# Performance work log

Measured on AMD Instinct MI355X. Metric: run time of the kernel, lower is better.

## Reference

```python
import jax, jax.numpy as jnp
import numpy as np

N, E, F_IN, H = 10000, 20000, 128, 8
C1, C2 = 512, 256          # per-head channels: head_dim1*8, head_dim2*8
B, OUT = 64, 10            # graphs per batch, output_dim


def _lin(k, fi, fo):
    return (jax.random.normal(k, (fi, fo), jnp.float32) / np.sqrt(fi)).astype(jnp.float32)


def setup_inputs() -> dict:
    key = jax.random.key(0)
    ks = jax.random.split(key, 24)
    inp = {
        "x": jax.random.normal(ks[0], (N, F_IN), jnp.float32),
        "edge_index": jax.random.randint(ks[1], (2, E), 0, N),
        "batch": jnp.sort(jax.random.randint(ks[2], (N,), 0, B)),
        # conv1 (in=F_IN, per-head C1, H heads)
        "Wq1": _lin(ks[3], F_IN, H * C1), "bq1": 0.01 * jax.random.normal(ks[4], (H * C1,)),
        "Wk1": _lin(ks[5], F_IN, H * C1), "bk1": 0.01 * jax.random.normal(ks[6], (H * C1,)),
        "Wv1": _lin(ks[7], F_IN, H * C1), "bv1": 0.01 * jax.random.normal(ks[8], (H * C1,)),
        "Ws1": _lin(ks[9], F_IN, C1), "bs1": 0.01 * jax.random.normal(ks[10], (C1,)),
        # conv2 (in=C1, per-head C2)
        "Wq2": _lin(ks[11], C1, H * C2), "bq2": 0.01 * jax.random.normal(ks[12], (H * C2,)),
        "Wk2": _lin(ks[13], C1, H * C2), "bk2": 0.01 * jax.random.normal(ks[14], (H * C2,)),
        "Wv2": _lin(ks[15], C1, H * C2), "bv2": 0.01 * jax.random.normal(ks[16], (H * C2,)),
        "Ws2": _lin(ks[17], C1, C2), "bs2": 0.01 * jax.random.normal(ks[18], (C2,)),
        # GlobalAttention gate and final fc
        "Wg": _lin(ks[19], C2, 1), "bg": jnp.zeros((1,), jnp.float32),
        "Wf": _lin(ks[20], C2, OUT), "bf": 0.01 * jax.random.normal(ks[21], (OUT,)),
    }
    return inp


def _segment_softmax(alpha, idx, n):
    # numerically-stable softmax over variable-size segments (PyG softmax)
    amax = jax.ops.segment_max(alpha, idx, num_segments=n)
    amax = jnp.where(jnp.isfinite(amax), amax, 0.0)
    e = jnp.exp(alpha - amax[idx])
    denom = jax.ops.segment_sum(e, idx, num_segments=n)
    return e / (denom[idx] + 1e-16)


def _transformer_conv(x, edge_index, Wq, bq, Wk, bk, Wv, bv, Ws, bs, C):
    n = x.shape[0]
    src, dst = edge_index[0], edge_index[1]  # message flows src -> dst
    q = (x @ Wq + bq).reshape(n, H, C)
    k = (x @ Wk + bk).reshape(n, H, C)
    v = (x @ Wv + bv).reshape(n, H, C)
    # per-edge multi-head attention logits [E, H]
    alpha = jnp.einsum('ehc,ehc->eh', q[dst], k[src]) / np.sqrt(C).astype(np.float32)
    a = _segment_softmax(alpha, dst, n)                       # [E, H]
    out = jax.ops.segment_sum(a[:, :, None] * v[src], dst, num_segments=n)  # [N, H, C]
    out = out.mean(axis=1)                                    # concat=False -> head mean
    return out + x @ Ws + bs                                  # root/skip connection


def reference(x, edge_index, batch,
              Wq1, bq1, Wk1, bk1, Wv1, bv1, Ws1, bs1,
              Wq2, bq2, Wk2, bk2, Wv2, bv2, Ws2, bs2,
              Wg, bg, Wf, bf):
    h = jax.nn.elu(_transformer_conv(x, edge_index, Wq1, bq1, Wk1, bk1, Wv1, bv1, Ws1, bs1, C1))
    h = jax.nn.elu(_transformer_conv(h, edge_index, Wq2, bq2, Wk2, bk2, Wv2, bv2, Ws2, bs2, C2))
    # GlobalAttention pooling: gate softmax within each graph, weighted sum
    gate = _segment_softmax((h @ Wg + bg)[:, 0], batch, B)    # [N]
    g = jax.ops.segment_sum(gate[:, None] * h, batch, num_segments=B)  # [B, C2]
    return g @ Wf + bf
```

## Files before the change

### kernel.cpp

```cpp
#include <hip/hip_runtime.h>
#include <math.h>

#define NN 10000
#define NE 20000
#define FIN 128
#define NHEAD 8
#define C1 512
#define C2 256
#define NB 64
#define NOUT 10

typedef _Float16 half8v __attribute__((ext_vector_type(8)));
typedef _Float16 half4v __attribute__((ext_vector_type(4)));
typedef _Float16 half2v __attribute__((ext_vector_type(2)));
typedef float f32x4 __attribute__((ext_vector_type(4)));

template<int VEC> struct VecT;
template<> struct VecT<2> { using T = half2v; };
template<> struct VecT<4> { using T = half4v; };
template<> struct VecT<8> { using T = half8v; };

__device__ __forceinline__ unsigned enc_f(float f) {
    unsigned u = __float_as_uint(f);
    return (u & 0x80000000u) ? ~u : (u | 0x80000000u);
}
__device__ __forceinline__ float dec_f(unsigned e) {
    return (e & 0x80000000u) ? __uint_as_float(e & 0x7fffffffu) : __uint_as_float(~e);
}

__global__ void cvt_f16(const float* __restrict__ in, _Float16* __restrict__ out, int n) {
    int i = blockIdx.x * blockDim.x + threadIdx.x;
    if (i < n) out[i] = (_Float16)in[i];
}

__global__ void transpose_cvt(const float* __restrict__ W, _Float16* __restrict__ Wt,
                              int K, int N) {
    __shared__ float tile[32][33];
    int n0 = blockIdx.x * 32, k0 = blockIdx.y * 32;
    int tx = threadIdx.x, ty = threadIdx.y;
    for (int j = ty; j < 32; j += 8) tile[j][tx] = W[(size_t)(k0 + j) * N + n0 + tx];
    __syncthreads();
    for (int j = ty; j < 32; j += 8)
        Wt[(size_t)(n0 + j) * K + k0 + tx] = (_Float16)tile[tx][j];
}

__global__ void transpose_stack(const float* __restrict__ Wv, _Float16* __restrict__ Bt,
                                int Cin, int Cout) {
    __shared__ float tile[32][33];
    int h = blockIdx.z;
    int c0 = blockIdx.x * 32, k0 = blockIdx.y * 32;
    int tx = threadIdx.x, ty = threadIdx.y;
    for (int j = ty; j < 32; j += 8)
        tile[j][tx] = Wv[(size_t)(k0 + j) * (NHEAD * Cout) + (size_t)h * Cout + c0 + tx];
    __syncthreads();
    for (int j = ty; j < 32; j += 8)
        Bt[(size_t)(c0 + j) * (NHEAD * Cin) + (size_t)h * Cin + k0 + tx] = (_Float16)tile[tx][j];
}

__global__ void bvmean_k(const float* __restrict__ bv, float* __restrict__ bvm, int C) {
    int c = blockIdx.x * blockDim.x + threadIdx.x;
    if (c >= C) return;
    float s = 0.f;
    #pragma unroll
    for (int h = 0; h < NHEAD; ++h) s += bv[h * C + c];
    bvm[c] = s * (1.0f / NHEAD);
}

__global__ void mstack_k(const _Float16* __restrict__ wtq1, const _Float16* __restrict__ wtk1,
                         _Float16* __restrict__ Mst) {
    int h = blockIdx.z;
    int i = blockIdx.x * 16 + threadIdx.x;
    int j = blockIdx.y * 16 + threadIdx.y;
    float acc = 0.f;
    for (int c = 0; c < C1; ++c)
        acc += (float)wtq1[((size_t)h * C1 + c) * FIN + i] *
               (float)wtk1[((size_t)h * C1 + c) * FIN + j];
    Mst[((size_t)h * FIN + j) * FIN + i] = (_Float16)acc;
}

__global__ void uvprep(const float* __restrict__ Wq1, const float* __restrict__ Wk1,
                       const float* __restrict__ bq1, const float* __restrict__ bk1,
                       float* __restrict__ u, float* __restrict__ v, float* __restrict__ ch) {
    int h = blockIdx.x, i = threadIdx.x;
    float su = 0.f, sv = 0.f;
    for (int c = 0; c < C1; ++c) {
        su += Wq1[(size_t)i * (NHEAD * C1) + h * C1 + c] * bk1[h * C1 + c];
        sv += Wk1[(size_t)i * (NHEAD * C1) + h * C1 + c] * bq1[h * C1 + c];
    }
    u[h * FIN + i] = su;
    v[h * FIN + i] = sv;
    if (i == 0) {
        float s = 0.f;
        for (int c = 0; c < C1; ++c) s += bq1[h * C1 + c] * bk1[h * C1 + c];
        ch[h] = s;
    }
}

__global__ void udvs_k(const _Float16* __restrict__ xb, const float* __restrict__ u,
                       const float* __restrict__ v, const float* __restrict__ ch,
                       float* __restrict__ ud, float* __restrict__ vs) {
    int idx = blockIdx.x * blockDim.x + threadIdx.x;
    if (idx >= NN * NHEAD) return;
    int n = idx >> 3, h = idx & 7;
    float su = ch[h], sv = 0.f;
    for (int i = 0; i < FIN; ++i) {
        float xv = (float)xb[(size_t)n * FIN + i];
        su += xv * u[h * FIN + i];
        sv += xv * v[h * FIN + i];
    }
    ud[idx] = su;
    vs[idx] = sv;
}

template<bool OUT_HALF, bool ACCUM>
__global__ __launch_bounds__(256) void gemm_tn(
    const _Float16* __restrict__ A, const _Float16* __restrict__ Bt,
    const float* __restrict__ bias, void* __restrict__ Cout, int ldc,
    int M, int K)
{
    __shared__ _Float16 As[128][40];
    __shared__ _Float16 Bs[128][40];
    const int t = threadIdx.x;
    const int m0 = blockIdx.y * 128, n0 = blockIdx.x * 128;
    const int w = t >> 6, lane = t & 63;
    const int wr = w >> 1, wc = w & 1;

    f32x4 acc[4][4];
    #pragma unroll
    for (int m = 0; m < 4; ++m)
        #pragma unroll
        for (int n = 0; n < 4; ++n)
            #pragma unroll
            for (int j = 0; j < 4; ++j) acc[m][n][j] = 0.f;

    for (int k0 = 0; k0 < K; k0 += 32) {
        #pragma unroll
        for (int i = 0; i < 2; ++i) {
            int c = t + i * 256;
            int row = c >> 2, kc = c & 3;
            int gr = m0 + row; gr = gr < M ? gr : M - 1;
            float4 va = *(const float4*)(A + (size_t)gr * K + k0 + kc * 8);
            *(float4*)(&As[row][kc * 8]) = va;
            float4 vb = *(const float4*)(Bt + (size_t)(n0 + row) * K + k0 + kc * 8);
            *(float4*)(&Bs[row][kc * 8]) = vb;
        }
        __syncthreads();
        half8v af[4], bf[4];
        #pragma unroll
        for (int m = 0; m < 4; ++m)
            af[m] = *(const half8v*)(&As[wr * 64 + m * 16 + (lane & 15)][(lane >> 4) * 8]);
        #pragma unroll
        for (int n = 0; n < 4; ++n)
            bf[n] = *(const half8v*)(&Bs[wc * 64 + n * 16 + (lane & 15)][(lane >> 4) * 8]);
        #pragma unroll
        for (int m = 0; m < 4; ++m)
            #pragma unroll
            for (int n = 0; n < 4; ++n)
                acc[m][n] = __builtin_amdgcn_mfma_f32_16x16x32_f16(af[m], bf[n], acc[m][n], 0, 0, 0);
        __syncthreads();
    }
    #pragma unroll
    for (int m = 0; m < 4; ++m) {
        int r0 = m0 + wr * 64 + m * 16 + (lane >> 4) * 4;
        #pragma unroll
        for (int n = 0; n < 4; ++n) {
            int col = n0 + wc * 64 + n * 16 + (lane & 15);
            float b = 0.f;
            if (!ACCUM) b = bias[col];
            #pragma unroll
            for (int r = 0; r < 4; ++r) {
                int row = r0 + r;
                if (row < M) {
                    float v = acc[m][n][r] + b;
                    if (ACCUM) v += ((float*)Cout)[(size_t)row * ldc + col];
                    if (OUT_HALF) ((_Float16*)Cout)[(size_t)row * ldc + col] = (_Float16)v;
                    else          ((float*)Cout)[(size_t)row * ldc + col] = v;
                }
            }
        }
    }
}

__global__ void zero_i32(int* __restrict__ p, int n) {
    int i = blockIdx.x * blockDim.x + threadIdx.x;
    if (i < n) p[i] = 0;
}
__global__ void hist_dst(const int* __restrict__ dst, int* __restrict__ deg) {
    int e = blockIdx.x * blockDim.x + threadIdx.x;
    if (e < NE) atomicAdd(&deg[dst[e]], 1);
}
__global__ void scan_deg(const int* __restrict__ deg, int* __restrict__ rowptr,
                         int* __restrict__ cursor, int n) {
    __shared__ int s[256];
    __shared__ int carry;
    int t = threadIdx.x;
    if (t == 0) carry = 0;
    __syncthreads();
    for (int base = 0; base < n; base += 256) {
        int v = (base + t < n) ? deg[base + t] : 0;
        s[t] = v;
        __syncthreads();
        for (int off = 1; off < 256; off <<= 1) {
            int x = (t >= off) ? s[t - off] : 0;
            __syncthreads();
            s[t] += x;
            __syncthreads();
        }
        int excl = carry + s[t] - v;
        if (base + t < n) { rowptr[base + t] = excl; cursor[base + t] = excl; }
        __syncthreads();
        if (t == 255) carry += s[255];
        __syncthreads();
    }
    if (t == 0) rowptr[n] = carry;
}
__global__ void scatter_edges(const int* __restrict__ dst, int* __restrict__ cursor,
                              int* __restrict__ eids) {
    int e = blockIdx.x * blockDim.x + threadIdx.x;
    if (e < NE) {
        int pos = atomicAdd(&cursor[dst[e]], 1);
        eids[pos] = e;
    }
}

__global__ void init_seg(unsigned* __restrict__ amax, float* __restrict__ denom, int n) {
    int i = blockIdx.x * blockDim.x + threadIdx.x;
    if (i < n) { amax[i] = 0x007FFFFFu; denom[i] = 0.f; }
}

__global__ void edge_alpha_lr(const _Float16* __restrict__ T, const _Float16* __restrict__ X,
                              const float* __restrict__ ud, const float* __restrict__ vs,
                              const int* __restrict__ src, const int* __restrict__ dst,
                              float* __restrict__ alpha, unsigned* __restrict__ amaxU,
                              float scale)
{
    int gi = blockIdx.x * blockDim.x + threadIdx.x;
    int e = gi >> 6, lane = threadIdx.x & 63;
    if (e >= NE) return;
    int s = src[e], d = dst[e];
    half2v xv = *(const half2v*)(X + (size_t)s * FIN + lane * 2);
    #pragma unroll
    for (int h = 0; h < NHEAD; ++h) {
        half2v tv = *(const half2v*)(T + ((size_t)d * NHEAD + h) * FIN + lane * 2);
        float sum = (float)tv[0] * (float)xv[0] + (float)tv[1] * (float)xv[1];
        #pragma unroll
        for (int off = 32; off; off >>= 1) sum += __shfl_xor(sum, off);
        if (lane == 0) {
            float al = (sum + ud[(size_t)d * NHEAD + h] + vs[(size_t)s * NHEAD + h]) * scale;
            alpha[(size_t)e * NHEAD + h] = al;
            atomicMax(&amaxU[(size_t)d * NHEAD + h], enc_f(al));
        }
    }
}

template<int C>
__global__ void edge_alpha_f(const _Float16* __restrict__ Q, const _Float16* __restrict__ Kh,
                             const int* __restrict__ src, const int* __restrict__ dst,
                             float* __restrict__ alpha, unsigned* __restrict__ amaxU,
                             float scale, int hbase, int G)
{
    constexpr int VEC = C / 64;
    using vecH = typename VecT<VEC>::T;
    int gi = blockIdx.x * blockDim.x + threadIdx.x;
    int e = gi >> 6, lane = threadIdx.x & 63;
    if (e >= NE) return;
    int s = src[e], d = dst[e];
    const _Float16* qp = Q + (size_t)d * ((size_t)G * C) + lane * VEC;
    const _Float16* kp = Kh + (size_t)s * ((size_t)G * C) + lane * VEC;
    for (int h = 0; h < G; ++h) {
        vecH q = *(const vecH*)(qp + h * C);
        vecH k = *(const vecH*)(kp + h * C);
        float sum = 0.f;
        #pragma unroll
        for (int j = 0; j < VEC; ++j) sum += (float)q[j] * (float)k[j];
        #pragma unroll
        for (int off = 32; off; off >>= 1) sum += __shfl_xor(sum, off);
        if (lane == 0) {
            float al = sum * scale;
            alpha[(size_t)e * NHEAD + hbase + h] = al;
            atomicMax(&amaxU[(size_t)d * NHEAD + hbase + h], enc_f(al));
        }
    }
}

__global__ void edge_expsum(const float* __restrict__ alpha, const int* __restrict__ dst,
                            const unsigned* __restrict__ amaxU,
                            float* __restrict__ ev, float* __restrict__ denom)
{
    int i = blockIdx.x * blockDim.x + threadIdx.x;
    if (i >= NE * NHEAD) return;
    int e = i >> 3, h = i & 7;
    int d = dst[e];
    float ex = expf(alpha[i] - dec_f(amaxU[(size_t)d * NHEAD + h]));
    ev[i] = ex;
    atomicAdd(&denom[(size_t)d * NHEAD + h], ex);
}

template<int C, int G>
__global__ void zaccum(const _Float16* __restrict__ X, const float* __restrict__ ev,
                       const float* __restrict__ denom, const int* __restrict__ rowptr,
                       const int* __restrict__ eids, const int* __restrict__ src,
                       _Float16* __restrict__ Z, int hbase)
{
    constexpr int VEC = C / 64;
    using vecH = typename VecT<VEC>::T;
    int gi = blockIdx.x * blockDim.x + threadIdx.x;
    int n = gi >> 6, lane = threadIdx.x & 63;
    if (n >= NN) return;
    int beg = rowptr[n], end = rowptr[n + 1];
    float rd[G];
    #pragma unroll
    for (int h = 0; h < G; ++h)
        rd[h] = (1.0f / NHEAD) / (denom[(size_t)n * NHEAD + hbase + h] + 1e-16f);
    float acc[G][VEC];
    #pragma unroll
    for (int h = 0; h < G; ++h)
        #pragma unroll
        for (int j = 0; j < VEC; ++j) acc[h][j] = 0.f;
    for (int i = beg; i < end; ++i) {
        int e = eids[i];
        int s = src[e];
        vecH xv = *(const vecH*)(X + (size_t)s * C + lane * VEC);
        #pragma unroll
        for (int h = 0; h < G; ++h) {
            float cf = ev[(size_t)e * NHEAD + hbase + h] * rd[h];
            #pragma unroll
            for (int j = 0; j < VEC; ++j) acc[h][j] += cf * (float)xv[j];
        }
    }
    #pragma unroll
    for (int h = 0; h < G; ++h) {
        vecH o;
        #pragma unroll
        for (int j = 0; j < VEC; ++j) o[j] = (_Float16)acc[h][j];
        *(vecH*)(Z + (size_t)n * (G * C) + (size_t)h * C + lane * VEC) = o;
    }
}

template<int C>
__global__ void node_aggr(const _Float16* __restrict__ V, const float* __restrict__ ev,
                          const float* __restrict__ denom, const int* __restrict__ rowptr,
                          const int* __restrict__ eids, const int* __restrict__ src,
                          float* __restrict__ acc, int hbase, int G)
{
    constexpr int VEC = C / 64;
    using vecH = typename VecT<VEC>::T;
    int gi = blockIdx.x * blockDim.x + threadIdx.x;
    int n = gi >> 6, lane = threadIdx.x & 63;
    if (n >= NN) return;
    int beg = rowptr[n], end = rowptr[n + 1];
    float a[VEC];
    #pragma unroll
    for (int j = 0; j < VEC; ++j) a[j] = 0.f;
    for (int h = 0; h < G; ++h) {
        float rd = 1.f / (denom[(size_t)n * NHEAD + hbase + h] + 1e-16f) * (1.f / NHEAD);
        for (int i = beg; i < end; ++i) {
            int e = eids[i];
            int s = src[e];
            float coeff = ev[(size_t)e * NHEAD + hbase + h] * rd;
            vecH v = *(const vecH*)(V + (size_t)s * ((size_t)G * C) + h * C + lane * VEC);
            #pragma unroll
            for (int j = 0; j < VEC; ++j) a[j] += coeff * (float)v[j];
        }
    }
    float* ap = acc + (size_t)n * C + lane * VEC;
    #pragma unroll
    for (int j = 0; j < VEC; ++j) ap[j] += a[j];
}

__global__ void elu_k(float* __restrict__ x, int n) {
    int i = blockIdx.x * blockDim.x + threadIdx.x;
    if (i < n) { float v = x[i]; x[i] = v > 0.f ? v : expm1f(v); }
}
__global__ void elu_cvt_bias(const float* __restrict__ in, _Float16* __restrict__ out,
                             const float* __restrict__ bvm, const int* __restrict__ deg,
                             int total) {
    int i = blockIdx.x * blockDim.x + threadIdx.x;
    if (i >= total) return;
    int c = i & (C1 - 1), n = i >> 9;
    float v = in[i] + (deg[n] > 0 ? bvm[c] : 0.f);
    v = v > 0.f ? v : expm1f(v);
    out[i] = (_Float16)v;
}

__global__ __launch_bounds__(256) void pool_fused(
    const float* __restrict__ H2, const float* __restrict__ Wg,
    const float* __restrict__ bg, const int* __restrict__ batch,
    const float* __restrict__ Wf, const float* __restrict__ bf,
    float* __restrict__ glogit, float* __restrict__ out)
{
    const int b = blockIdx.x;
    const int t = threadIdx.x, lane = t & 63, w = t >> 6;
    __shared__ int sbeg, send;
    __shared__ float sred[4];
    if (t == 0) {
        int lo = 0, hi = NN;
        while (lo < hi) { int mid = (lo + hi) >> 1; if (batch[mid] < b) lo = mid + 1; else hi = mid; }
        sbeg = lo;
        hi = NN;
        while (lo < hi) { int mid = (lo + hi) >> 1; if (batch[mid] < b + 1) lo = mid + 1; else hi = mid; }
        send = lo;
    }
    __syncthreads();
    const int beg = sbeg, end = send;
    const float bg0 = bg[0];

    float lmax = -INFINITY;
    for (int n = beg + w; n < end; n += 4) {
        float4 h = ((const float4*)(H2 + (size_t)n * C2))[lane];
        float4 wv = ((const float4*)Wg)[lane];
        float sum = h.x * wv.x + h.y * wv.y + h.z * wv.z + h.w * wv.w;
        #pragma unroll
        for (int off = 32; off; off >>= 1) sum += __shfl_xor(sum, off);
        sum += bg0;
        if (lane == 0) glogit[n] = sum;
        lmax = fmaxf(lmax, sum);
    }
    if (lane == 0) sred[w] = lmax;
    __syncthreads();
    float m = fmaxf(fmaxf(sred[0], sred[1]), fmaxf(sred[2], sred[3]));
    if (!isfinite(m)) m = 0.f;
    __syncthreads();

    float ls = 0.f;
    for (int n = beg + t; n < end; n += 256) {
        float e = expf(glogit[n] - m);
        glogit[n] = e;
        ls += e;
    }
    #pragma unroll
    for (int off = 32; off; off >>= 1) ls += __shfl_xor(ls, off);
    if (lane == 0) sred[w] = ls;
    __syncthreads();
    const float denom = sred[0] + sred[1] + sred[2] + sred[3] + 1e-16f;
    __syncthreads();

    float acc = 0.f;
    for (int n = beg; n < end; ++n)
        acc += glogit[n] * H2[(size_t)n * C2 + t];
    const float gc = acc / denom;

    for (int o = 0; o < NOUT; ++o) {
        float p = gc * Wf[t * NOUT + o];
        #pragma unroll
        for (int off = 32; off; off >>= 1) p += __shfl_xor(p, off);
        __syncthreads();
        if (lane == 0) sred[w] = p;
        __syncthreads();
        if (t == 0) out[b * NOUT + o] = sred[0] + sred[1] + sred[2] + sred[3] + bf[o];
    }
}

extern "C" void kernel_launch(void* const* d_in, const int* in_sizes, int n_in,
                              void* d_out, int out_size, void* d_ws, size_t ws_size,
                              hipStream_t stream) {
    (void)in_sizes; (void)n_in; (void)out_size; (void)ws_size;
    const float* x     = (const float*)d_in[0];
    const int*   ei    = (const int*)  d_in[1];
    const int*   batch = (const int*)  d_in[2];
    const float* Wq1 = (const float*)d_in[3];  const float* bq1 = (const float*)d_in[4];
    const float* Wk1 = (const float*)d_in[5];  const float* bk1 = (const float*)d_in[6];
    const float* Wv1 = (const float*)d_in[7];  const float* bv1 = (const float*)d_in[8];
    const float* Ws1 = (const float*)d_in[9];  const float* bs1 = (const float*)d_in[10];
    const float* Wq2 = (const float*)d_in[11]; const float* bq2 = (const float*)d_in[12];
    const float* Wk2 = (const float*)d_in[13]; const float* bk2 = (const float*)d_in[14];
    const float* Wv2 = (const float*)d_in[15]; const float* bv2 = (const float*)d_in[16];
    const float* Ws2 = (const float*)d_in[17]; const float* bs2 = (const float*)d_in[18];
    const float* Wg  = (const float*)d_in[19]; const float* bg  = (const float*)d_in[20];
    const float* Wf  = (const float*)d_in[21]; const float* bf  = (const float*)d_in[22];

    const int* src = ei;
    const int* dst = ei + NE;

    char* base = (char*)d_ws;
    size_t off = 0;
    auto alloc = [&](size_t bytes) -> char* {
        char* p = base + off;
        off = (off + bytes + 255) & ~(size_t)255;
        return p;
    };
    _Float16* xb   = (_Float16*)alloc((size_t)NN * FIN * 2);
    _Float16* wtq1 = (_Float16*)alloc((size_t)NHEAD * C1 * FIN * 2);
    _Float16* wtk1 = (_Float16*)alloc((size_t)NHEAD * C1 * FIN * 2);
    _Float16* bvs1 = (_Float16*)alloc((size_t)C1 * NHEAD * FIN * 2);
    _Float16* wts1 = (_Float16*)alloc((size_t)C1 * FIN * 2);
    _Float16* wtq2 = (_Float16*)alloc((size_t)NHEAD * C2 * C1 * 2);
    _Float16* wtk2 = (_Float16*)alloc((size_t)NHEAD * C2 * C1 * 2);
    _Float16* wtv2 = (_Float16*)alloc((size_t)NHEAD * C2 * C1 * 2);
    _Float16* wts2 = (_Float16*)alloc((size_t)C2 * C1 * 2);
    _Float16* Mst  = (_Float16*)alloc((size_t)NHEAD * FIN * FIN * 2);
    float* uvecs = (float*)alloc((size_t)NHEAD * FIN * 4);
    float* vvecs = (float*)alloc((size_t)NHEAD * FIN * 4);
    float* chd   = (float*)alloc((size_t)NHEAD * 4);
    float* ud    = (float*)alloc((size_t)NN * NHEAD * 4);
    float* vs    = (float*)alloc((size_t)NN * NHEAD * 4);
    float* zbias = (float*)alloc((size_t)NHEAD * FIN * 4);
    float* acc1 = (float*)alloc((size_t)NN * C1 * 4);
    _Float16* h1b = (_Float16*)alloc((size_t)NN * C1 * 2);
    float* alpha = (float*)alloc((size_t)NE * NHEAD * 4);
    float* ev    = (float*)alloc((size_t)NE * NHEAD * 4);
    unsigned* amaxU = (unsigned*)alloc((size_t)NN * NHEAD * 4);
    float* denom = (float*)alloc((size_t)NN * NHEAD * 4);
    int* deg    = (int*)alloc((size_t)NN * 4);
    int* rowptr = (int*)alloc((size_t)(NN + 1) * 4);
    int* cursor = (int*)alloc((size_t)NN * 4);
    int* eids   = (int*)alloc((size_t)NE * 4);
    float* bvm1 = (float*)alloc((size_t)C1 * 4);
    _Float16* Tbuf = (_Float16*)alloc((size_t)NN * NHEAD * FIN * 2);
    _Float16* Qbuf = (_Float16*)alloc((size_t)NN * NHEAD * C2 * 2);
    _Float16* Kbuf = (_Float16*)alloc((size_t)NN * NHEAD * C2 * 2);
    _Float16* Zbuf = Qbuf;
    _Float16* Vbuf = Qbuf;
    float* acc2 = acc1;

    const dim3 blk(256);
    const float sc1 = 1.0f / sqrtf((float)C1);
    const float sc2 = 1.0f / sqrtf((float)C2);
    const int edge_blocks = (NE * 64) / 256;
    const int node_blocks = (NN * 64) / 256;
    const int gy = (NN + 127) / 128;

    cvt_f16<<<((size_t)NN * FIN + 255) / 256, blk, 0, stream>>>(x, xb, NN * FIN);
    {
        dim3 tb(32, 8);
        transpose_cvt<<<dim3(NHEAD * C1 / 32, FIN / 32), tb, 0, stream>>>(Wq1, wtq1, FIN, NHEAD * C1);
        transpose_cvt<<<dim3(NHEAD * C1 / 32, FIN / 32), tb, 0, stream>>>(Wk1, wtk1, FIN, NHEAD * C1);
        transpose_stack<<<dim3(C1 / 32, FIN / 32, NHEAD), tb, 0, stream>>>(Wv1, bvs1, FIN, C1);
        transpose_cvt<<<dim3(C1 / 32, FIN / 32),         tb, 0, stream>>>(Ws1, wts1, FIN, C1);
        transpose_cvt<<<dim3(NHEAD * C2 / 32, C1 / 32),  tb, 0, stream>>>(Wq2, wtq2, C1, NHEAD * C2);
        transpose_cvt<<<dim3(NHEAD * C2 / 32, C1 / 32),  tb, 0, stream>>>(Wk2, wtk2, C1, NHEAD * C2);
        transpose_cvt<<<dim3(NHEAD * C2 / 32, C1 / 32),  tb, 0, stream>>>(Wv2, wtv2, C1, NHEAD * C2);
        transpose_cvt<<<dim3(C2 / 32, C1 / 32),          tb, 0, stream>>>(Ws2, wts2, C1, C2);
    }
    bvmean_k<<<(C1 + 255) / 256, blk, 0, stream>>>(bv1, bvm1, C1);
    mstack_k<<<dim3(FIN / 16, FIN / 16, NHEAD), dim3(16, 16), 0, stream>>>(wtq1, wtk1, Mst);
    uvprep<<<NHEAD, FIN, 0, stream>>>(Wq1, Wk1, bq1, bk1, uvecs, vvecs, chd);
    udvs_k<<<(NN * NHEAD + 255) / 256, blk, 0, stream>>>(xb, uvecs, vvecs, chd, ud, vs);
    zero_i32<<<(NHEAD * FIN + 255) / 256, blk, 0, stream>>>((int*)zbias, NHEAD * FIN);

    zero_i32<<<(NN + 255) / 256, blk, 0, stream>>>(deg, NN);
    hist_dst<<<(NE + 255) / 256, blk, 0, stream>>>(dst, deg);
    scan_deg<<<1, blk, 0, stream>>>(deg, rowptr, cursor, NN);
    scatter_edges<<<(NE + 255) / 256, blk, 0, stream>>>(dst, cursor, eids);

    gemm_tn<false, false><<<dim3(C1 / 128, gy), blk, 0, stream>>>(
        xb, wts1, bs1, acc1, C1, NN, FIN);
    gemm_tn<true, false><<<dim3(NHEAD * FIN / 128, gy), blk, 0, stream>>>(
        xb, Mst, zbias, Tbuf, NHEAD * FIN, NN, FIN);
    init_seg<<<(NN * NHEAD + 255) / 256, blk, 0, stream>>>(amaxU, denom, NN * NHEAD);
    edge_alpha_lr<<<edge_blocks, blk, 0, stream>>>(Tbuf, xb, ud, vs, src, dst,
                                                   alpha, amaxU, sc1);
    edge_expsum<<<(NE * NHEAD + 255) / 256, blk, 0, stream>>>(alpha, dst, amaxU, ev, denom);
    zaccum<FIN, NHEAD><<<node_blocks, blk, 0, stream>>>(xb, ev, denom, rowptr, eids, src,
                                                        Zbuf, 0);
    gemm_tn<false, true><<<dim3(C1 / 128, gy), blk, 0, stream>>>(
        Zbuf, bvs1, nullptr, acc1, C1, NN, NHEAD * FIN);
    elu_cvt_bias<<<((size_t)NN * C1 + 255) / 256, blk, 0, stream>>>(
        acc1, h1b, bvm1, deg, NN * C1);

    gemm_tn<false, false><<<dim3(C2 / 128, gy), blk, 0, stream>>>(
        h1b, wts2, bs2, acc2, C2, NN, C1);
    init_seg<<<(NN * NHEAD + 255) / 256, blk, 0, stream>>>(amaxU, denom, NN * NHEAD);
    gemm_tn<true, false><<<dim3(NHEAD * C2 / 128, gy), blk, 0, stream>>>(
        h1b, wtq2, bq2, Qbuf, NHEAD * C2, NN, C1);
    gemm_tn<true, false><<<dim3(NHEAD * C2 / 128, gy), blk, 0, stream>>>(
        h1b, wtk2, bk2, Kbuf, NHEAD * C2, NN, C1);
    edge_alpha_f<C2><<<edge_blocks, blk, 0, stream>>>(Qbuf, Kbuf, src, dst, alpha, amaxU,
                                                      sc2, 0, NHEAD);
    edge_expsum<<<(NE * NHEAD + 255) / 256, blk, 0, stream>>>(alpha, dst, amaxU, ev, denom);
    gemm_tn<true, false><<<dim3(NHEAD * C2 / 128, gy), blk, 0, stream>>>(
        h1b, wtv2, bv2, Vbuf, NHEAD * C2, NN, C1);
    node_aggr<C2><<<node_blocks, blk, 0, stream>>>(Vbuf, ev, denom, rowptr, eids, src,
                                                   acc2, 0, NHEAD);
    elu_k<<<((size_t)NN * C2 + 255) / 256, blk, 0, stream>>>(acc2, NN * C2);

    pool_fused<<<NB, blk, 0, stream>>>(acc2, Wg, bg, batch, Wf, bf, alpha, (float*)d_out);
}
```

Measured before the change: 686.0 us.

## Fuse conv2 Q/K/V projections into one GEMM and use direct global-to-LDS loads

Concatenates the transposed Wq2/Wk2/Wv2 weights and biases so a single GEMM writes an interleaved QKV buffer, and the edge-alpha and aggregation kernels read it through a row stride. The GEMM tile loads switch from register-staged float4 copies to the global_load_lds builtin with an unpadded LDS layout. The conv1 skip GEMM is also moved later in the stream. The intent is fewer launches, one pass over h1b for all three projections, and less register traffic in the load phase. The costs are a larger strided QKV buffer with worse locality in the gathers, and possible LDS bank conflicts now that the padding is gone.

```diff
diff --git a/kernel.cpp b/kernel.cpp
--- a/kernel.cpp
+++ b/kernel.cpp
@@ -28,6 +28,12 @@
     return (e & 0x80000000u) ? __uint_as_float(e & 0x7fffffffu) : __uint_as_float(~e);
 }
 
+__device__ __forceinline__ void gload16(const _Float16* g, _Float16* l) {
+    __builtin_amdgcn_global_load_lds(
+        (const __attribute__((address_space(1))) unsigned int*)(const void*)g,
+        (__attribute__((address_space(3))) unsigned int*)(void*)l, 16, 0, 0);
+}
+
 __global__ void cvt_f16(const float* __restrict__ in, _Float16* __restrict__ out, int n) {
     int i = blockIdx.x * blockDim.x + threadIdx.x;
     if (i < n) out[i] = (_Float16)in[i];
@@ -64,6 +70,15 @@
     #pragma unroll
     for (int h = 0; h < NHEAD; ++h) s += bv[h * C + c];
     bvm[c] = s * (1.0f / NHEAD);
+}
+
+__global__ void concat_bias3(const float* __restrict__ a, const float* __restrict__ b,
+                             const float* __restrict__ c, float* __restrict__ o) {
+    int i = blockIdx.x * blockDim.x + threadIdx.x;
+    const int n = NHEAD * C2;
+    if (i < n) o[i] = a[i];
+    else if (i < 2 * n) o[i] = b[i - n];
+    else if (i < 3 * n) o[i] = c[i - 2 * n];
 }
 
 __global__ void mstack_k(const _Float16* __restrict__ wtq1, const _Float16* __restrict__ wtk1,
@@ -118,12 +133,13 @@
     const float* __restrict__ bias, void* __restrict__ Cout, int ldc,
     int M, int K)
 {
-    __shared__ _Float16 As[128][40];
-    __shared__ _Float16 Bs[128][40];
+    __shared__ _Float16 As[128 * 32];
+    __shared__ _Float16 Bs[128 * 32];
     const int t = threadIdx.x;
     const int m0 = blockIdx.y * 128, n0 = blockIdx.x * 128;
     const int w = t >> 6, lane = t & 63;
     const int wr = w >> 1, wc = w & 1;
+    const int r_lo = lane >> 2, slot = lane & 3;
 
     f32x4 acc[4][4];
     #pragma unroll
@@ -136,22 +152,20 @@
     for (int k0 = 0; k0 < K; k0 += 32) {
         #pragma unroll
         for (int i = 0; i < 2; ++i) {
-            int c = t + i * 256;
-            int row = c >> 2, kc = c & 3;
+            int chunk = 2 * w + i;
+            int row = chunk * 16 + r_lo;
             int gr = m0 + row; gr = gr < M ? gr : M - 1;
-            float4 va = *(const float4*)(A + (size_t)gr * K + k0 + kc * 8);
-            *(float4*)(&As[row][kc * 8]) = va;
-            float4 vb = *(const float4*)(Bt + (size_t)(n0 + row) * K + k0 + kc * 8);
-            *(float4*)(&Bs[row][kc * 8]) = vb;
+            gload16(A + (size_t)gr * K + k0 + slot * 8, &As[chunk * 512]);
+            gload16(Bt + (size_t)(n0 + row) * K + k0 + slot * 8, &Bs[chunk * 512]);
         }
         __syncthreads();
         half8v af[4], bf[4];
         #pragma unroll
         for (int m = 0; m < 4; ++m)
-            af[m] = *(const half8v*)(&As[wr * 64 + m * 16 + (lane & 15)][(lane >> 4) * 8]);
+            af[m] = *(const half8v*)(&As[(wr * 64 + m * 16 + (lane & 15)) * 32 + (lane >> 4) * 8]);
         #pragma unroll
         for (int n = 0; n < 4; ++n)
-            bf[n] = *(const half8v*)(&Bs[wc * 64 + n * 16 + (lane & 15)][(lane >> 4) * 8]);
+            bf[n] = *(const half8v*)(&Bs[(wc * 64 + n * 16 + (lane & 15)) * 32 + (lane >> 4) * 8]);
         #pragma unroll
         for (int m = 0; m < 4; ++m)
             #pragma unroll
@@ -255,7 +269,7 @@
 
 template<int C>
 __global__ void edge_alpha_f(const _Float16* __restrict__ Q, const _Float16* __restrict__ Kh,
-                             const int* __restrict__ src, const int* __restrict__ dst,
+                             int ldq, const int* __restrict__ src, const int* __restrict__ dst,
                              float* __restrict__ alpha, unsigned* __restrict__ amaxU,
                              float scale, int hbase, int G)
 {
@@ -265,8 +279,8 @@
     int e = gi >> 6, lane = threadIdx.x & 63;
     if (e >= NE) return;
     int s = src[e], d = dst[e];
-    const _Float16* qp = Q + (size_t)d * ((size_t)G * C) + lane * VEC;
-    const _Float16* kp = Kh + (size_t)s * ((size_t)G * C) + lane * VEC;
+    const _Float16* qp = Q + (size_t)d * ldq + lane * VEC;
+    const _Float16* kp = Kh + (size_t)s * ldq + lane * VEC;
     for (int h = 0; h < G; ++h) {
         vecH q = *(const vecH*)(qp + h * C);
         vecH k = *(const vecH*)(kp + h * C);
@@ -338,10 +352,11 @@
 }
 
 template<int C>
-__global__ void node_aggr(const _Float16* __restrict__ V, const float* __restrict__ ev,
-                          const float* __restrict__ denom, const int* __restrict__ rowptr,
-                          const int* __restrict__ eids, const int* __restrict__ src,
-                          float* __restrict__ acc, int hbase, int G)
+__global__ void node_aggr(const _Float16* __restrict__ V, int ldv,
+                          const float* __restrict__ ev, const float* __restrict__ denom,
+                          const int* __restrict__ rowptr, const int* __restrict__ eids,
+                          const int* __restrict__ src, float* __restrict__ acc,
+                          int hbase, int G)
 {
     constexpr int VEC = C / 64;
     using vecH = typename VecT<VEC>::T;
@@ -358,7 +373,7 @@
             int e = eids[i];
             int s = src[e];
             float coeff = ev[(size_t)e * NHEAD + hbase + h] * rd;
-            vecH v = *(const vecH*)(V + (size_t)s * ((size_t)G * C) + h * C + lane * VEC);
+            vecH v = *(const vecH*)(V + (size_t)s * ldv + h * C + lane * VEC);
             #pragma unroll
             for (int j = 0; j < VEC; ++j) a[j] += coeff * (float)v[j];
         }
@@ -479,23 +494,22 @@
         off = (off + bytes + 255) & ~(size_t)255;
         return p;
     };
-    _Float16* xb   = (_Float16*)alloc((size_t)NN * FIN * 2);
-    _Float16* wtq1 = (_Float16*)alloc((size_t)NHEAD * C1 * FIN * 2);
-    _Float16* wtk1 = (_Float16*)alloc((size_t)NHEAD * C1 * FIN * 2);
-    _Float16* bvs1 = (_Float16*)alloc((size_t)C1 * NHEAD * FIN * 2);
-    _Float16* wts1 = (_Float16*)alloc((size_t)C1 * FIN * 2);
-    _Float16* wtq2 = (_Float16*)alloc((size_t)NHEAD * C2 * C1 * 2);
-    _Float16* wtk2 = (_Float16*)alloc((size_t)NHEAD * C2 * C1 * 2);
-    _Float16* wtv2 = (_Float16*)alloc((size_t)NHEAD * C2 * C1 * 2);
-    _Float16* wts2 = (_Float16*)alloc((size_t)C2 * C1 * 2);
-    _Float16* Mst  = (_Float16*)alloc((size_t)NHEAD * FIN * FIN * 2);
+    _Float16* xb    = (_Float16*)alloc((size_t)NN * FIN * 2);
+    _Float16* wtq1  = (_Float16*)alloc((size_t)NHEAD * C1 * FIN * 2);
+    _Float16* wtk1  = (_Float16*)alloc((size_t)NHEAD * C1 * FIN * 2);
+    _Float16* bvs1  = (_Float16*)alloc((size_t)C1 * NHEAD * FIN * 2);
+    _Float16* wts1  = (_Float16*)alloc((size_t)C1 * FIN * 2);
+    _Float16* wqkv2 = (_Float16*)alloc((size_t)3 * NHEAD * C2 * C1 * 2);
+    _Float16* wts2  = (_Float16*)alloc((size_t)C2 * C1 * 2);
+    _Float16* Mst   = (_Float16*)alloc((size_t)NHEAD * FIN * FIN * 2);
     float* uvecs = (float*)alloc((size_t)NHEAD * FIN * 4);
     float* vvecs = (float*)alloc((size_t)NHEAD * FIN * 4);
     float* chd   = (float*)alloc((size_t)NHEAD * 4);
     float* ud    = (float*)alloc((size_t)NN * NHEAD * 4);
     float* vs    = (float*)alloc((size_t)NN * NHEAD * 4);
     float* zbias = (float*)alloc((size_t)NHEAD * FIN * 4);
-    float* acc1 = (float*)alloc((size_t)NN * C1 * 4);
+    float* bqkv2 = (float*)alloc((size_t)3 * NHEAD * C2 * 4);
+    float* acc1  = (float*)alloc((size_t)NN * C1 * 4);
     _Float16* h1b = (_Float16*)alloc((size_t)NN * C1 * 2);
     float* alpha = (float*)alloc((size_t)NE * NHEAD * 4);
     float* ev    = (float*)alloc((size_t)NE * NHEAD * 4);
@@ -506,12 +520,11 @@
     int* cursor = (int*)alloc((size_t)NN * 4);
     int* eids   = (int*)alloc((size_t)NE * 4);
     float* bvm1 = (float*)alloc((size_t)C1 * 4);
-    _Float16* Tbuf = (_Float16*)alloc((size_t)NN * NHEAD * FIN * 2);
-    _Float16* Qbuf = (_Float16*)alloc((size_t)NN * NHEAD * C2 * 2);
-    _Float16* Kbuf = (_Float16*)alloc((size_t)NN * NHEAD * C2 * 2);
-    _Float16* Zbuf = Qbuf;
-    _Float16* Vbuf = Qbuf;
+    _Float16* Tbuf   = (_Float16*)alloc((size_t)NN * NHEAD * FIN * 2);
+    _Float16* QKVbuf = (_Float16*)alloc((size_t)NN * 3 * NHEAD * C2 * 2);
+    _Float16* Zbuf = QKVbuf;
     float* acc2 = acc1;
+    const int LDQKV = 3 * NHEAD * C2;
 
     const dim3 blk(256);
     const float sc1 = 1.0f / sqrtf((float)C1);
@@ -527,9 +540,11 @@
         transpose_cvt<<<dim3(NHEAD * C1 / 32, FIN / 32), tb, 0, stream>>>(Wk1, wtk1, FIN, NHEAD * C1);
         transpose_stack<<<dim3(C1 / 32, FIN / 32, NHEAD), tb, 0, stream>>>(Wv1, bvs1, FIN, C1);
         transpose_cvt<<<dim3(C1 / 32, FIN / 32),         tb, 0, stream>>>(Ws1, wts1, FIN, C1);
-        transpose_cvt<<<dim3(NHEAD * C2 / 32, C1 / 32),  tb, 0, stream>>>(Wq2, wtq2, C1, NHEAD * C2);
-        transpose_cvt<<<dim3(NHEAD * C2 / 32, C1 / 32),  tb, 0, stream>>>(Wk2, wtk2, C1, NHEAD * C2);
-        transpose_cvt<<<dim3(NHEAD * C2 / 32, C1 / 32),  tb, 0, stream>>>(Wv2, wtv2, C1, NHEAD * C2);
+        transpose_cvt<<<dim3(NHEAD * C2 / 32, C1 / 32),  tb, 0, stream>>>(Wq2, wqkv2, C1, NHEAD * C2);
+        transpose_cvt<<<dim3(NHEAD * C2 / 32, C1 / 32),  tb, 0, stream>>>(
+            Wk2, wqkv2 + (size_t)NHEAD * C2 * C1, C1, NHEAD * C2);
+        transpose_cvt<<<dim3(NHEAD * C2 / 32, C1 / 32),  tb, 0, stream>>>(
+            Wv2, wqkv2 + (size_t)2 * NHEAD * C2 * C1, C1, NHEAD * C2);
         transpose_cvt<<<dim3(C2 / 32, C1 / 32),          tb, 0, stream>>>(Ws2, wts2, C1, C2);
     }
     bvmean_k<<<(C1 + 255) / 256, blk, 0, stream>>>(bv1, bvm1, C1);
@@ -537,20 +552,21 @@
     uvprep<<<NHEAD, FIN, 0, stream>>>(Wq1, Wk1, bq1, bk1, uvecs, vvecs, chd);
     udvs_k<<<(NN * NHEAD + 255) / 256, blk, 0, stream>>>(xb, uvecs, vvecs, chd, ud, vs);
     zero_i32<<<(NHEAD * FIN + 255) / 256, blk, 0, stream>>>((int*)zbias, NHEAD * FIN);
+    concat_bias3<<<(3 * NHEAD * C2 + 255) / 256, blk, 0, stream>>>(bq2, bk2, bv2, bqkv2);
 
     zero_i32<<<(NN + 255) / 256, blk, 0, stream>>>(deg, NN);
     hist_dst<<<(NE + 255) / 256, blk, 0, stream>>>(dst, deg);
     scan_deg<<<1, blk, 0, stream>>>(deg, rowptr, cursor, NN);
     scatter_edges<<<(NE + 255) / 256, blk, 0, stream>>>(dst, cursor, eids);
 
-    gemm_tn<false, false><<<dim3(C1 / 128, gy), blk, 0, stream>>>(
-        xb, wts1, bs1, acc1, C1, NN, FIN);
     gemm_tn<true, false><<<dim3(NHEAD * FIN / 128, gy), blk, 0, stream>>>(
         xb, Mst, zbias, Tbuf, NHEAD * FIN, NN, FIN);
     init_seg<<<(NN * NHEAD + 255) / 256, blk, 0, stream>>>(amaxU, denom, NN * NHEAD);
     edge_alpha_lr<<<edge_blocks, blk, 0, stream>>>(Tbuf, xb, ud, vs, src, dst,
                                                    alpha, amaxU, sc1);
     edge_expsum<<<(NE * NHEAD + 255) / 256, blk, 0, stream>>>(alpha, dst, amaxU, ev, denom);
+    gemm_tn<false, false><<<dim3(C1 / 128, gy), blk, 0, stream>>>(
+        xb, wts1, bs1, acc1, C1, NN, FIN);
     zaccum<FIN, NHEAD><<<node_blocks, blk, 0, stream>>>(xb, ev, denom, rowptr, eids, src,
                                                         Zbuf, 0);
     gemm_tn<false, true><<<dim3(C1 / 128, gy), blk, 0, stream>>>(
@@ -561,17 +577,13 @@
     gemm_tn<false, false><<<dim3(C2 / 128, gy), blk, 0, stream>>>(
         h1b, wts2, bs2, acc2, C2, NN, C1);
     init_seg<<<(NN * NHEAD + 255) / 256, blk, 0, stream>>>(amaxU, denom, NN * NHEAD);
-    gemm_tn<true, false><<<dim3(NHEAD * C2 / 128, gy), blk, 0, stream>>>(
-        h1b, wtq2, bq2, Qbuf, NHEAD * C2, NN, C1);
-    gemm_tn<true, false><<<dim3(NHEAD * C2 / 128, gy), blk, 0, stream>>>(
-        h1b, wtk2, bk2, Kbuf, NHEAD * C2, NN, C1);
-    edge_alpha_f<C2><<<edge_blocks, blk, 0, stream>>>(Qbuf, Kbuf, src, dst, alpha, amaxU,
-                                                      sc2, 0, NHEAD);
+    gemm_tn<true, false><<<dim3(LDQKV / 128, gy), blk, 0, stream>>>(
+        h1b, wqkv2, bqkv2, QKVbuf, LDQKV, NN, C1);
+    edge_alpha_f<C2><<<edge_blocks, blk, 0, stream>>>(
+        QKVbuf, QKVbuf + NHEAD * C2, LDQKV, src, dst, alpha, amaxU, sc2, 0, NHEAD);
     edge_expsum<<<(NE * NHEAD + 255) / 256, blk, 0, stream>>>(alpha, dst, amaxU, ev, denom);
-    gemm_tn<true, false><<<dim3(NHEAD * C2 / 128, gy), blk, 0, stream>>>(
-        h1b, wtv2, bv2, Vbuf, NHEAD * C2, NN, C1);
-    node_aggr<C2><<<node_blocks, blk, 0, stream>>>(Vbuf, ev, denom, rowptr, eids, src,
-                                                   acc2, 0, NHEAD);
+    node_aggr<C2><<<node_blocks, blk, 0, stream>>>(
+        QKVbuf + 2 * NHEAD * C2, LDQKV, ev, denom, rowptr, eids, src, acc2, 0, NHEAD);
     elu_k<<<((size_t)NN * C2 + 255) / 256, blk, 0, stream>>>(acc2, NN * C2);
 
     pool_fused<<<NB, blk, 0, stream>>>(acc2, Wg, bg, batch, Wf, bf, alpha, (float*)d_out);
```

Result: faster. 656.2 us (-4.3%).
